# Optimization experiments

Measured on AMD Instinct MI355X. Metric: run time of the kernel, lower is better.

Reference implementation:

```python
import jax, jax.numpy as jnp
import numpy as np

DIM = 1024
NUM_HEADS = 16
HEAD_DIM = DIM // NUM_HEADS
SCALE = HEAD_DIM ** -0.5


def setup_inputs() -> dict:
    key = jax.random.key(0)
    ks = jax.random.split(key, 6)
    B, N, C = 2, 2048, DIM
    std = 1.0 / np.sqrt(C)
    x = jax.random.normal(ks[0], (B, N, C), dtype=jnp.float32)
    wq = jax.random.normal(ks[1], (C, C), dtype=jnp.float32) * std
    wk = jax.random.normal(ks[2], (C, C), dtype=jnp.float32) * std
    wv = jax.random.normal(ks[3], (C, C), dtype=jnp.float32) * std
    w_proj = jax.random.normal(ks[4], (C, C), dtype=jnp.float32) * std
    b_proj = jax.random.normal(ks[5], (C,), dtype=jnp.float32) * 0.01
    return {"x": x, "wq": wq, "wk": wk, "wv": wv, "w_proj": w_proj, "b_proj": b_proj}


def reference(x, wq, wk, wv, w_proj, b_proj):
    B, N, C = x.shape
    H, D = NUM_HEADS, HEAD_DIM
    Nq = N // 2
    # q from first half of tokens; k, v from all tokens
    q = (x[:, :Nq] @ wq.T).reshape(B, Nq, H, D).transpose(0, 2, 1, 3)  # [B,H,Nq,D]
    k = (x @ wk.T).reshape(B, N, H, D).transpose(0, 2, 1, 3)           # [B,H,N,D]
    v = (x @ wv.T).reshape(B, N, H, D).transpose(0, 2, 1, 3)           # [B,H,N,D]
    attn = jnp.einsum('bhqd,bhkd->bhqk', q, k) * SCALE
    attn = jax.nn.softmax(attn, axis=-1)
    out = jnp.einsum('bhqk,bhkd->bhqd', attn, v)                       # [B,H,Nq,D]
    out = out.transpose(0, 2, 1, 3).reshape(B, Nq, C)
    return out @ w_proj.T + b_proj
```

## Files before the change

### kernel.cpp

```cpp
#include <hip/hip_runtime.h>

typedef _Float16 f16;
typedef _Float16 f16x8 __attribute__((ext_vector_type(8)));
typedef _Float16 f16x4 __attribute__((ext_vector_type(4)));
typedef float f32x4 __attribute__((ext_vector_type(4)));

#define MFMA_F16(a, b, c) __builtin_amdgcn_mfma_f32_16x16x32_f16(a, b, c, 0, 0, 0)

__device__ __forceinline__ void gld16(const void* g, void* l) {
  __builtin_amdgcn_global_load_lds(
      (const __attribute__((address_space(1))) unsigned int*)(unsigned long long)g,
      (__attribute__((address_space(3))) unsigned int*)(unsigned long long)l, 16, 0, 0);
}

__global__ __launch_bounds__(256) void cvt_x_kernel(const float* __restrict__ in,
                                                    f16* __restrict__ out, int n8) {
  int i = blockIdx.x * 256 + threadIdx.x;
  if (i >= n8) return;
  const float4* p = (const float4*)(in + (size_t)i * 8);
  float4 a = p[0], b = p[1];
  f16x8 o = {(f16)a.x, (f16)a.y, (f16)a.z, (f16)a.w,
             (f16)b.x, (f16)b.y, (f16)b.z, (f16)b.w};
  *(f16x8*)(out + (size_t)i * 8) = o;
}

__global__ __launch_bounds__(256) void cvt_w4_kernel(const float* __restrict__ w0,
                                                     const float* __restrict__ w1,
                                                     const float* __restrict__ w2,
                                                     const float* __restrict__ w3,
                                                     f16* __restrict__ out) {
  int i = blockIdx.x * 256 + threadIdx.x;
  int t = i >> 17, r = i & 131071;
  const float* w = (t == 0) ? w0 : (t == 1) ? w1 : (t == 2) ? w2 : w3;
  const float4* p = (const float4*)(w + (size_t)r * 8);
  float4 a = p[0], b = p[1];
  f16x8 o = {(f16)a.x, (f16)a.y, (f16)a.z, (f16)a.w,
             (f16)b.x, (f16)b.y, (f16)b.z, (f16)b.w};
  *(f16x8*)(out + (size_t)t * 1048576 + (size_t)r * 8) = o;
}

__global__ __launch_bounds__(256) void qkv_gemm_kernel(
    const f16* __restrict__ A, const f16* __restrict__ Wq,
    const f16* __restrict__ Wk, const f16* __restrict__ Wv,
    f16* __restrict__ Qo, f16* __restrict__ Ko, f16* __restrict__ VT) {
  __shared__ __align__(16) f16 As[2][128 * 64];
  __shared__ __align__(16) f16 Bs[2][128 * 64];
  const int bid = blockIdx.x + blockIdx.y * 8;
  const int swz = (bid & 7) * 80 + (bid >> 3);
  const int bx = swz & 7, y = swz >> 3;
  const f16* Bw;
  f16* Co = nullptr;
  int mt, isv = 0;
  if (y < 16) { Bw = Wq; Co = Qo; mt = (y & 7) | ((y >> 3) << 4); }
  else if (y < 48) { Bw = Wk; Co = Ko; mt = y - 16; }
  else { Bw = Wv; isv = 1; mt = y - 48; }
  const int m0 = mt * 128, n0 = bx * 128;
  const int tid = threadIdx.x, lane = tid & 63, w = tid >> 6;
  const int wr = w >> 1, wc = w & 1, g = lane >> 4, c = lane & 15;
  const int r_st = tid >> 3, t_st = tid & 7;

  auto stage = [&](int k0, int buf) {
#pragma unroll
    for (int i = 0; i < 4; ++i) {
      int row = r_st + i * 32;
      int sl = (t_st ^ (row & 7)) * 8;
      gld16(&A[(size_t)(m0 + row) * 1024 + k0 + sl], &As[buf][(row * 8 + t_st) * 8]);
      gld16(&Bw[(size_t)(n0 + row) * 1024 + k0 + sl], &Bs[buf][(row * 8 + t_st) * 8]);
    }
  };

  f32x4 acc[4][4] = {};

  stage(0, 0);
  __syncthreads();

  for (int t = 0; t < 16; ++t) {
    const int cur = t & 1;
    if (t < 15) stage((t + 1) * 64, cur ^ 1);
#pragma unroll
    for (int kb = 0; kb < 2; ++kb) {
      f16x8 af[4], bf[4];
#pragma unroll
      for (int m2 = 0; m2 < 4; ++m2)
        af[m2] = *(const f16x8*)&As[cur][(wr * 64 + m2 * 16 + c) * 64 +
                                         (((kb * 4 + g) ^ (c & 7)) * 8)];
#pragma unroll
      for (int nt = 0; nt < 4; ++nt)
        bf[nt] = *(const f16x8*)&Bs[cur][(wc * 64 + nt * 16 + c) * 64 +
                                         (((kb * 4 + g) ^ (c & 7)) * 8)];
#pragma unroll
      for (int m2 = 0; m2 < 4; ++m2)
#pragma unroll
        for (int nt = 0; nt < 4; ++nt)
          acc[m2][nt] = MFMA_F16(af[m2], bf[nt], acc[m2][nt]);
    }
    __syncthreads();
  }

  if (isv) {
    const int b = m0 >> 11;
    const int n_base = (m0 & 2047) + wr * 64 + g * 4;
#pragma unroll
    for (int m2 = 0; m2 < 4; ++m2)
#pragma unroll
      for (int nt = 0; nt < 4; ++nt) {
        int col = n0 + wc * 64 + nt * 16 + c;
        int h = col >> 6, d = col & 63;
        f16x4 pv = {(f16)acc[m2][nt][0], (f16)acc[m2][nt][1],
                    (f16)acc[m2][nt][2], (f16)acc[m2][nt][3]};
        *(f16x4*)&VT[((size_t)((b * 16 + h) * 64 + d)) * 2048 + n_base + m2 * 16] = pv;
      }
  } else {
#pragma unroll
    for (int m2 = 0; m2 < 4; ++m2)
#pragma unroll
      for (int nt = 0; nt < 4; ++nt) {
        int col = n0 + wc * 64 + nt * 16 + c;
#pragma unroll
        for (int r = 0; r < 4; ++r)
          Co[(size_t)(m0 + wr * 64 + m2 * 16 + g * 4 + r) * 1024 + col] =
              (f16)acc[m2][nt][r];
      }
  }
}

__global__ __launch_bounds__(256) void proj_gemm_kernel(
    const f16* __restrict__ A, const f16* __restrict__ Bw,
    float* __restrict__ C, const float* __restrict__ bias) {
  __shared__ __align__(16) f16 As[2][64 * 64];
  __shared__ __align__(16) f16 Bs[2][64 * 64];
  const int bid = blockIdx.x + blockIdx.y * 16;
  const int swz = (bid & 7) * 64 + (bid >> 3);
  const int m0 = (swz >> 4) * 64, n0 = (swz & 15) * 64;
  const int tid = threadIdx.x, lane = tid & 63, w = tid >> 6;
  const int wr = w >> 1, wc = w & 1, g = lane >> 4, c = lane & 15;
  const int r_st = tid >> 3, t_st = tid & 7;

  auto stage = [&](int k0, int buf) {
#pragma unroll
    for (int i = 0; i < 2; ++i) {
      int row = r_st + i * 32;
      int sl = (t_st ^ (row & 7)) * 8;
      gld16(&A[(size_t)(m0 + row) * 1024 + k0 + sl], &As[buf][(row * 8 + t_st) * 8]);
      gld16(&Bw[(size_t)(n0 + row) * 1024 + k0 + sl], &Bs[buf][(row * 8 + t_st) * 8]);
    }
  };

  f32x4 acc[2][2] = {};

  stage(0, 0);
  __syncthreads();

  for (int t = 0; t < 16; ++t) {
    const int cur = t & 1;
    if (t < 15) stage((t + 1) * 64, cur ^ 1);
#pragma unroll
    for (int kb = 0; kb < 2; ++kb) {
      f16x8 af[2], bf[2];
#pragma unroll
      for (int m2 = 0; m2 < 2; ++m2)
        af[m2] = *(const f16x8*)&As[cur][(wr * 32 + m2 * 16 + c) * 64 +
                                         (((kb * 4 + g) ^ (c & 7)) * 8)];
#pragma unroll
      for (int nt = 0; nt < 2; ++nt)
        bf[nt] = *(const f16x8*)&Bs[cur][(wc * 32 + nt * 16 + c) * 64 +
                                         (((kb * 4 + g) ^ (c & 7)) * 8)];
#pragma unroll
      for (int m2 = 0; m2 < 2; ++m2)
#pragma unroll
        for (int nt = 0; nt < 2; ++nt)
          acc[m2][nt] = MFMA_F16(af[m2], bf[nt], acc[m2][nt]);
    }
    __syncthreads();
  }

#pragma unroll
  for (int m2 = 0; m2 < 2; ++m2)
#pragma unroll
    for (int nt = 0; nt < 2; ++nt) {
      int col = n0 + wc * 32 + nt * 16 + c;
      float bv = bias[col];
#pragma unroll
      for (int r = 0; r < 4; ++r)
        C[(size_t)(m0 + wr * 32 + m2 * 16 + g * 4 + r) * 1024 + col] =
            acc[m2][nt][r] + bv;
    }
}

__global__ __launch_bounds__(256, 3) void attn_kernel(const f16* __restrict__ Q,
                                                      const f16* __restrict__ Kg,
                                                      const f16* __restrict__ VT,
                                                      f16* __restrict__ Opart,
                                                      float* __restrict__ ML) {
  __shared__ __align__(16) f16 Ks[2][64 * 64];
  __shared__ __align__(16) f16 Vs[64 * 64];
  __shared__ __align__(16) f16 Ps[4][32 * 64];
  const int flat = blockIdx.x;
  const int swz = (flat & 7) * 128 + (flat >> 3);
  const int qt = swz & 7, h = (swz >> 3) & 15;
  const int ch = (swz >> 7) & 3, b = swz >> 9;
  const int tid = threadIdx.x, lane = tid & 63, w = tid >> 6;
  const int g = lane >> 4, c = lane & 15;
  const int r_st = tid >> 3, t_st = tid & 7;

  const f16* Kbase = Kg + (size_t)(b * 2048 + ch * 512) * 1024 + h * 64;
  const f16* Vbase = VT + ((size_t)((b * 16 + h) * 64)) * 2048 + ch * 512;

  f16x8 qf[2][2];
#pragma unroll
  for (int qs = 0; qs < 2; ++qs) {
    const f16* qp =
        Q + (size_t)(b * 2048 + qt * 128 + w * 32 + qs * 16 + c) * 1024 + h * 64;
    qf[qs][0] = *(const f16x8*)(qp + g * 8);
    qf[qs][1] = *(const f16x8*)(qp + 32 + g * 8);
#pragma unroll
    for (int j = 0; j < 8; ++j) {
      qf[qs][0][j] = (f16)((float)qf[qs][0][j] * 0.1803368801f);
      qf[qs][1][j] = (f16)((float)qf[qs][1][j] * 0.1803368801f);
    }
  }

  auto stageK = [&](int t, int buf) {
#pragma unroll
    for (int i = 0; i < 2; ++i) {
      int row = r_st + i * 32;
      int sl = (t_st ^ (row & 7)) * 8;
      gld16(&Kbase[(size_t)(t * 64 + row) * 1024 + sl],
            &Ks[buf][(row * 8 + t_st) * 8]);
    }
  };
  auto stageV = [&](int t) {
#pragma unroll
    for (int i = 0; i < 2; ++i) {
      int row = r_st + i * 32;
      int sl = (t_st ^ (row & 7)) * 8;
      gld16(&Vbase[(size_t)row * 2048 + t * 64 + sl], &Vs[(row * 8 + t_st) * 8]);
    }
  };

  f32x4 oaccT[4][2] = {};
  float l_part[2] = {0.f, 0.f};

  stageK(0, 0);
  stageV(0);
  asm volatile("s_waitcnt vmcnt(0)" ::: "memory");
  __builtin_amdgcn_s_barrier();
  __builtin_amdgcn_sched_barrier(0);

  for (int t = 0; t < 8; ++t) {
    const int cur = t & 1;
    if (t < 7) stageK(t + 1, cur ^ 1);

#pragma unroll
    for (int qs = 0; qs < 2; ++qs) {
      f32x4 s[4] = {};
#pragma unroll
      for (int kt = 0; kt < 4; ++kt) {
        f16x8 kf0 =
            *(const f16x8*)&Ks[cur][(kt * 16 + c) * 64 + ((g ^ (c & 7)) * 8)];
        f16x8 kf1 =
            *(const f16x8*)&Ks[cur][(kt * 16 + c) * 64 + (((4 + g) ^ (c & 7)) * 8)];
        s[kt] = MFMA_F16(kf0, qf[qs][0], s[kt]);
        s[kt] = MFMA_F16(kf1, qf[qs][1], s[kt]);
      }
      float rs = 0.f;
#pragma unroll
      for (int kt = 0; kt < 4; ++kt)
#pragma unroll
        for (int r = 0; r < 4; ++r) {
          float p = exp2f(s[kt][r]);
          s[kt][r] = p;
          rs += p;
        }
      l_part[qs] += rs;
#pragma unroll
      for (int kt = 0; kt < 4; ++kt) {
        f16x4 pv = {(f16)s[kt][0], (f16)s[kt][1], (f16)s[kt][2], (f16)s[kt][3]};
        *(f16x4*)&Ps[w][(qs * 16 + c) * 64 +
                        (((kt * 2 + (g >> 1)) ^ (c & 7)) * 8) + (g & 1) * 4] = pv;
      }
    }

    if (t < 7) {
      asm volatile("s_waitcnt vmcnt(2)" ::: "memory");
    } else {
      asm volatile("s_waitcnt vmcnt(0)" ::: "memory");
    }
    __builtin_amdgcn_s_barrier();
    __builtin_amdgcn_sched_barrier(0);

#pragma unroll
    for (int kb = 0; kb < 2; ++kb) {
      f16x8 pf0 =
          *(const f16x8*)&Ps[w][c * 64 + (((kb * 4 + g) ^ (c & 7)) * 8)];
      f16x8 pf1 =
          *(const f16x8*)&Ps[w][(16 + c) * 64 + (((kb * 4 + g) ^ (c & 7)) * 8)];
#pragma unroll
      for (int dt = 0; dt < 4; ++dt) {
        f16x8 vf = *(const f16x8*)&Vs[(dt * 16 + c) * 64 +
                                      (((kb * 4 + g) ^ (c & 7)) * 8)];
        oaccT[dt][0] = MFMA_F16(vf, pf0, oaccT[dt][0]);
        oaccT[dt][1] = MFMA_F16(vf, pf1, oaccT[dt][1]);
      }
    }

    asm volatile("s_waitcnt vmcnt(0)" ::: "memory");
    __builtin_amdgcn_s_barrier();
    __builtin_amdgcn_sched_barrier(0);
    if (t < 7) stageV(t + 1);
  }

  float lf[2];
#pragma unroll
  for (int qs = 0; qs < 2; ++qs) {
    float l = l_part[qs];
    l += __shfl_xor(l, 16);
    l += __shfl_xor(l, 32);
    lf[qs] = l;
  }
#pragma unroll
  for (int qs = 0; qs < 2; ++qs) {
    float li = 1.f / lf[qs];
#pragma unroll
    for (int dt = 0; dt < 4; ++dt) {
      f16x4 ov = {(f16)(oaccT[dt][qs][0] * li), (f16)(oaccT[dt][qs][1] * li),
                  (f16)(oaccT[dt][qs][2] * li), (f16)(oaccT[dt][qs][3] * li)};
      *(f16x4*)&Opart[(size_t)ch * 2097152 +
                      (size_t)(b * 1024 + qt * 128 + w * 32 + qs * 16 + c) * 1024 +
                      h * 64 + dt * 16 + g * 4] = ov;
    }
  }
  if (lane < 16) {
#pragma unroll
    for (int qs = 0; qs < 2; ++qs)
      ML[ch * 32768 + (b * 1024 + qt * 128 + w * 32 + qs * 16 + lane) * 16 + h] =
          lf[qs];
  }
}

__global__ __launch_bounds__(256) void combine_kernel(const f16* __restrict__ Opart,
                                                      const float* __restrict__ ML,
                                                      f16* __restrict__ O16) {
  int i = blockIdx.x * 256 + threadIdx.x;
  int row = i >> 7;
  int h = (i & 127) >> 3;
  float l0 = ML[row * 16 + h];
  float l1 = ML[32768 + row * 16 + h];
  float l2 = ML[65536 + row * 16 + h];
  float l3 = ML[98304 + row * 16 + h];
  float inv = 1.f / (l0 + l1 + l2 + l3);
  f16x8 o0 = *(const f16x8*)&Opart[(size_t)i * 8];
  f16x8 o1 = *(const f16x8*)&Opart[2097152 + (size_t)i * 8];
  f16x8 o2 = *(const f16x8*)&Opart[4194304 + (size_t)i * 8];
  f16x8 o3 = *(const f16x8*)&Opart[6291456 + (size_t)i * 8];
  f16x8 r;
#pragma unroll
  for (int j = 0; j < 8; ++j)
    r[j] = (f16)((l0 * (float)o0[j] + l1 * (float)o1[j] + l2 * (float)o2[j] +
                  l3 * (float)o3[j]) * inv);
  *(f16x8*)&O16[(size_t)i * 8] = r;
}

extern "C" void kernel_launch(void* const* d_in, const int* in_sizes, int n_in,
                              void* d_out, int out_size, void* d_ws, size_t ws_size,
                              hipStream_t stream) {
  const float* x = (const float*)d_in[0];
  const float* wq = (const float*)d_in[1];
  const float* wk = (const float*)d_in[2];
  const float* wv = (const float*)d_in[3];
  const float* wp = (const float*)d_in[4];
  const float* bp = (const float*)d_in[5];
  float* out = (float*)d_out;

  char* p = (char*)d_ws;
  f16* x16 = (f16*)p;   p += (size_t)4194304 * 2;
  f16* w16 = (f16*)p;   p += (size_t)4 * 1048576 * 2;
  f16* Q16 = (f16*)p;   p += (size_t)4194304 * 2;
  f16* K16 = (f16*)p;   p += (size_t)4194304 * 2;
  f16* VT16 = (f16*)p;  p += (size_t)4194304 * 2;
  f16* Opart = (f16*)p; p += (size_t)8388608 * 2;
  f16* O16 = (f16*)p;   p += (size_t)2097152 * 2;

  f16* wq16 = w16;
  f16* wk16 = w16 + 1048576;
  f16* wv16 = w16 + 2 * 1048576;
  f16* wp16 = w16 + 3 * 1048576;

  cvt_x_kernel<<<4194304 / 8 / 256, 256, 0, stream>>>(x, x16, 4194304 / 8);
  cvt_w4_kernel<<<4 * 131072 / 256, 256, 0, stream>>>(wq, wk, wv, wp, w16);

  qkv_gemm_kernel<<<dim3(8, 80), 256, 0, stream>>>(x16, wq16, wk16, wv16, Q16, K16,
                                                   VT16);

  float* MLp = (float*)x16;
  attn_kernel<<<dim3(1024), 256, 0, stream>>>(Q16, K16, VT16, Opart, MLp);
  combine_kernel<<<1024, 256, 0, stream>>>(Opart, MLp, O16);

  proj_gemm_kernel<<<dim3(16, 32), 256, 0, stream>>>(O16, wp16, out, bp);
}
```

Baseline: 95.89 us.

## Shrink QKV GEMM M-tile, split-K proj GEMM with atomics, prioritize attention MFMAs

The QKV GEMM now uses a 64-row M tile, doubling the grid to 1280 blocks so more CUs are busy. The projection GEMM splits K into two halves and accumulates with float atomics; the combine kernel pre-fills the output with the bias. The attention kernel raises wave priority around its MFMA blocks with s_setprio. The trade-offs are less operand reuse per tile in the QKV GEMM, plus atomic traffic and an extra bias write pass for the projection.

```diff
diff --git a/kernel.cpp b/kernel.cpp
--- a/kernel.cpp
+++ b/kernel.cpp
@@ -43,33 +43,38 @@
     const f16* __restrict__ A, const f16* __restrict__ Wq,
     const f16* __restrict__ Wk, const f16* __restrict__ Wv,
     f16* __restrict__ Qo, f16* __restrict__ Ko, f16* __restrict__ VT) {
-  __shared__ __align__(16) f16 As[2][128 * 64];
+  __shared__ __align__(16) f16 As[2][64 * 64];
   __shared__ __align__(16) f16 Bs[2][128 * 64];
   const int bid = blockIdx.x + blockIdx.y * 8;
-  const int swz = (bid & 7) * 80 + (bid >> 3);
+  const int swz = (bid & 7) * 160 + (bid >> 3);
   const int bx = swz & 7, y = swz >> 3;
   const f16* Bw;
   f16* Co = nullptr;
   int mt, isv = 0;
-  if (y < 16) { Bw = Wq; Co = Qo; mt = (y & 7) | ((y >> 3) << 4); }
-  else if (y < 48) { Bw = Wk; Co = Ko; mt = y - 16; }
-  else { Bw = Wv; isv = 1; mt = y - 48; }
-  const int m0 = mt * 128, n0 = bx * 128;
+  if (y < 32) { Bw = Wq; Co = Qo; mt = (y & 15) | ((y >> 4) << 5); }
+  else if (y < 96) { Bw = Wk; Co = Ko; mt = y - 32; }
+  else { Bw = Wv; isv = 1; mt = y - 96; }
+  const int m0 = mt * 64, n0 = bx * 128;
   const int tid = threadIdx.x, lane = tid & 63, w = tid >> 6;
   const int wr = w >> 1, wc = w & 1, g = lane >> 4, c = lane & 15;
   const int r_st = tid >> 3, t_st = tid & 7;
 
   auto stage = [&](int k0, int buf) {
 #pragma unroll
+    for (int i = 0; i < 2; ++i) {
+      int row = r_st + i * 32;
+      int sl = (t_st ^ (row & 7)) * 8;
+      gld16(&A[(size_t)(m0 + row) * 1024 + k0 + sl], &As[buf][(row * 8 + t_st) * 8]);
+    }
+#pragma unroll
     for (int i = 0; i < 4; ++i) {
       int row = r_st + i * 32;
       int sl = (t_st ^ (row & 7)) * 8;
-      gld16(&A[(size_t)(m0 + row) * 1024 + k0 + sl], &As[buf][(row * 8 + t_st) * 8]);
       gld16(&Bw[(size_t)(n0 + row) * 1024 + k0 + sl], &Bs[buf][(row * 8 + t_st) * 8]);
     }
   };
 
-  f32x4 acc[4][4] = {};
+  f32x4 acc[2][4] = {};
 
   stage(0, 0);
   __syncthreads();
@@ -79,17 +84,16 @@
     if (t < 15) stage((t + 1) * 64, cur ^ 1);
 #pragma unroll
     for (int kb = 0; kb < 2; ++kb) {
-      f16x8 af[4], bf[4];
-#pragma unroll
-      for (int m2 = 0; m2 < 4; ++m2)
-        af[m2] = *(const f16x8*)&As[cur][(wr * 64 + m2 * 16 + c) * 64 +
-                                         (((kb * 4 + g) ^ (c & 7)) * 8)];
+      f16x8 af[2], bf[4];
+      const int sw = ((kb * 4 + g) ^ (c & 7)) * 8;
+#pragma unroll
+      for (int m2 = 0; m2 < 2; ++m2)
+        af[m2] = *(const f16x8*)&As[cur][(wr * 32 + m2 * 16 + c) * 64 + sw];
 #pragma unroll
       for (int nt = 0; nt < 4; ++nt)
-        bf[nt] = *(const f16x8*)&Bs[cur][(wc * 64 + nt * 16 + c) * 64 +
-                                         (((kb * 4 + g) ^ (c & 7)) * 8)];
-#pragma unroll
-      for (int m2 = 0; m2 < 4; ++m2)
+        bf[nt] = *(const f16x8*)&Bs[cur][(wc * 64 + nt * 16 + c) * 64 + sw];
+#pragma unroll
+      for (int m2 = 0; m2 < 2; ++m2)
 #pragma unroll
         for (int nt = 0; nt < 4; ++nt)
           acc[m2][nt] = MFMA_F16(af[m2], bf[nt], acc[m2][nt]);
@@ -99,9 +103,9 @@
 
   if (isv) {
     const int b = m0 >> 11;
-    const int n_base = (m0 & 2047) + wr * 64 + g * 4;
-#pragma unroll
-    for (int m2 = 0; m2 < 4; ++m2)
+    const int n_base = (m0 & 2047) + wr * 32 + g * 4;
+#pragma unroll
+    for (int m2 = 0; m2 < 2; ++m2)
 #pragma unroll
       for (int nt = 0; nt < 4; ++nt) {
         int col = n0 + wc * 64 + nt * 16 + c;
@@ -112,13 +116,13 @@
       }
   } else {
 #pragma unroll
-    for (int m2 = 0; m2 < 4; ++m2)
+    for (int m2 = 0; m2 < 2; ++m2)
 #pragma unroll
       for (int nt = 0; nt < 4; ++nt) {
         int col = n0 + wc * 64 + nt * 16 + c;
 #pragma unroll
         for (int r = 0; r < 4; ++r)
-          Co[(size_t)(m0 + wr * 64 + m2 * 16 + g * 4 + r) * 1024 + col] =
+          Co[(size_t)(m0 + wr * 32 + m2 * 16 + g * 4 + r) * 1024 + col] =
               (f16)acc[m2][nt][r];
       }
   }
@@ -126,12 +130,13 @@
 
 __global__ __launch_bounds__(256) void proj_gemm_kernel(
     const f16* __restrict__ A, const f16* __restrict__ Bw,
-    float* __restrict__ C, const float* __restrict__ bias) {
+    float* __restrict__ C) {
   __shared__ __align__(16) f16 As[2][64 * 64];
   __shared__ __align__(16) f16 Bs[2][64 * 64];
-  const int bid = blockIdx.x + blockIdx.y * 16;
-  const int swz = (bid & 7) * 64 + (bid >> 3);
-  const int m0 = (swz >> 4) * 64, n0 = (swz & 15) * 64;
+  const int bid = blockIdx.x;
+  const int swz = (bid & 7) * 128 + (bid >> 3);
+  const int n0 = (swz & 15) * 64, m0 = ((swz >> 4) & 31) * 64;
+  const int kbase = (swz >> 9) * 512;
   const int tid = threadIdx.x, lane = tid & 63, w = tid >> 6;
   const int wr = w >> 1, wc = w & 1, g = lane >> 4, c = lane & 15;
   const int r_st = tid >> 3, t_st = tid & 7;
@@ -148,23 +153,22 @@
 
   f32x4 acc[2][2] = {};
 
-  stage(0, 0);
+  stage(kbase, 0);
   __syncthreads();
 
-  for (int t = 0; t < 16; ++t) {
+  for (int t = 0; t < 8; ++t) {
     const int cur = t & 1;
-    if (t < 15) stage((t + 1) * 64, cur ^ 1);
+    if (t < 7) stage(kbase + (t + 1) * 64, cur ^ 1);
 #pragma unroll
     for (int kb = 0; kb < 2; ++kb) {
       f16x8 af[2], bf[2];
+      const int sw = ((kb * 4 + g) ^ (c & 7)) * 8;
 #pragma unroll
       for (int m2 = 0; m2 < 2; ++m2)
-        af[m2] = *(const f16x8*)&As[cur][(wr * 32 + m2 * 16 + c) * 64 +
-                                         (((kb * 4 + g) ^ (c & 7)) * 8)];
+        af[m2] = *(const f16x8*)&As[cur][(wr * 32 + m2 * 16 + c) * 64 + sw];
 #pragma unroll
       for (int nt = 0; nt < 2; ++nt)
-        bf[nt] = *(const f16x8*)&Bs[cur][(wc * 32 + nt * 16 + c) * 64 +
-                                         (((kb * 4 + g) ^ (c & 7)) * 8)];
+        bf[nt] = *(const f16x8*)&Bs[cur][(wc * 32 + nt * 16 + c) * 64 + sw];
 #pragma unroll
       for (int m2 = 0; m2 < 2; ++m2)
 #pragma unroll
@@ -179,11 +183,10 @@
 #pragma unroll
     for (int nt = 0; nt < 2; ++nt) {
       int col = n0 + wc * 32 + nt * 16 + c;
-      float bv = bias[col];
 #pragma unroll
       for (int r = 0; r < 4; ++r)
-        C[(size_t)(m0 + wr * 32 + m2 * 16 + g * 4 + r) * 1024 + col] =
-            acc[m2][nt][r] + bv;
+        unsafeAtomicAdd(&C[(size_t)(m0 + wr * 32 + m2 * 16 + g * 4 + r) * 1024 + col],
+                        acc[m2][nt][r]);
     }
 }
 
@@ -254,6 +257,7 @@
 #pragma unroll
     for (int qs = 0; qs < 2; ++qs) {
       f32x4 s[4] = {};
+      __builtin_amdgcn_s_setprio(1);
 #pragma unroll
       for (int kt = 0; kt < 4; ++kt) {
         f16x8 kf0 =
@@ -263,6 +267,7 @@
         s[kt] = MFMA_F16(kf0, qf[qs][0], s[kt]);
         s[kt] = MFMA_F16(kf1, qf[qs][1], s[kt]);
       }
+      __builtin_amdgcn_s_setprio(0);
       float rs = 0.f;
 #pragma unroll
       for (int kt = 0; kt < 4; ++kt)
@@ -289,6 +294,7 @@
     __builtin_amdgcn_s_barrier();
     __builtin_amdgcn_sched_barrier(0);
 
+    __builtin_amdgcn_s_setprio(1);
 #pragma unroll
     for (int kb = 0; kb < 2; ++kb) {
       f16x8 pf0 =
@@ -303,6 +309,7 @@
         oaccT[dt][1] = MFMA_F16(vf, pf1, oaccT[dt][1]);
       }
     }
+    __builtin_amdgcn_s_setprio(0);
 
     asm volatile("s_waitcnt vmcnt(0)" ::: "memory");
     __builtin_amdgcn_s_barrier();
@@ -340,7 +347,9 @@
 
 __global__ __launch_bounds__(256) void combine_kernel(const f16* __restrict__ Opart,
                                                       const float* __restrict__ ML,
-                                                      f16* __restrict__ O16) {
+                                                      f16* __restrict__ O16,
+                                                      float* __restrict__ outp,
+                                                      const float* __restrict__ bias) {
   int i = blockIdx.x * 256 + threadIdx.x;
   int row = i >> 7;
   int h = (i & 127) >> 3;
@@ -359,6 +368,9 @@
     r[j] = (f16)((l0 * (float)o0[j] + l1 * (float)o1[j] + l2 * (float)o2[j] +
                   l3 * (float)o3[j]) * inv);
   *(f16x8*)&O16[(size_t)i * 8] = r;
+  int cb = (i & 127) * 8;
+#pragma unroll
+  for (int j = 0; j < 8; ++j) outp[(size_t)i * 8 + j] = bias[cb + j];
 }
 
 extern "C" void kernel_launch(void* const* d_in, const int* in_sizes, int n_in,
@@ -389,12 +401,12 @@
   cvt_x_kernel<<<4194304 / 8 / 256, 256, 0, stream>>>(x, x16, 4194304 / 8);
   cvt_w4_kernel<<<4 * 131072 / 256, 256, 0, stream>>>(wq, wk, wv, wp, w16);
 
-  qkv_gemm_kernel<<<dim3(8, 80), 256, 0, stream>>>(x16, wq16, wk16, wv16, Q16, K16,
-                                                   VT16);
+  qkv_gemm_kernel<<<dim3(8, 160), 256, 0, stream>>>(x16, wq16, wk16, wv16, Q16, K16,
+                                                    VT16);
 
   float* MLp = (float*)x16;
   attn_kernel<<<dim3(1024), 256, 0, stream>>>(Q16, K16, VT16, Opart, MLp);
-  combine_kernel<<<1024, 256, 0, stream>>>(Opart, MLp, O16);
-
-  proj_gemm_kernel<<<dim3(16, 32), 256, 0, stream>>>(O16, wp16, out, bp);
-}
+  combine_kernel<<<1024, 256, 0, stream>>>(Opart, MLp, O16, out, bp);
+
+  proj_gemm_kernel<<<dim3(1024), 256, 0, stream>>>(O16, wp16, out);
+}
```

New measurement: 99.98 us. +4.3%, slower.
